# Performance work log

Measured on AMD Instinct MI355X. Metric: run time of the kernel, lower is better.

Reference implementation:

```python
import jax, jax.numpy as jnp
import numpy as np

# QuantumConv2d from ESPCN-PyTorch (quantum variant).
# QuantumLinear(kH, kW, ...) is a parameterized quantum circuit mapping a flattened
# kH*kW patch to kH Z-expectation values. We model the standard single-qubit-per-row
# RY-chain circuit: out[k] = cos( sum_w patch[k, w] + theta[k] )  (Z expectation after
# sequential RY rotations by the kW row inputs plus one trainable angle per row).
# The conv then averages the kH outputs and sums over input channels, exactly as the
# torch forward does. We replicate the original's circuits[i*j] indexing (i=out ch,
# j=in ch), and use cos(a+b)=cos a cos b - sin a sin b to turn the channel/row
# reduction into two dense einsums (same math, efficient expression).

KH, KW = 3, 3
PH, PW = 1, 1
OC = 32


def setup_inputs() -> dict:
    key = jax.random.key(0)
    k1, k2 = jax.random.split(key)
    x = jax.random.normal(k1, (8, 16, 128, 128), dtype=jnp.float32)
    # one circuit per (out_ch, in_ch, kernel_row): oC*iC*kH = 32*16*3 = 1536, kH params each
    theta = jax.random.normal(k2, (OC * 16 * KH, KH), dtype=jnp.float32)
    return {"x": x, "theta": theta}


def _row_window_sums(x):
    # x: (n, iC, H, W) -> (n, iC, kH, oH, oW): sum over the kW window for each kernel row
    xp = jnp.pad(x, ((0, 0), (0, 0), (PH, PH), (PW, PW)))
    Hp, Wp = xp.shape[2], xp.shape[3]
    oH, oW = Hp - (KH - 1), Wp - (KW - 1)
    rows = []
    for k in range(KH):  # tiny fixed loop over kernel rows
        s = xp[:, :, k:k + oH, 0:oW]
        for w in range(1, KW):
            s = s + xp[:, :, k:k + oH, w:w + oW]
        rows.append(s)
    return jnp.stack(rows, axis=2)


def reference(x, theta):
    n, iC = x.shape[0], x.shape[1]
    R = _row_window_sums(x)  # (n, iC, kH, oH, oW) angle sums per patch row
    # replicate torch's self.circuits[i * j] lookup
    idx = jnp.arange(OC)[:, None] * jnp.arange(iC)[None, :]  # (oC, iC)
    th = theta[idx]  # (oC, iC, kH)
    # out[n,i,h,w] = sum_j mean_k cos(R[n,j,k,h,w] + th[i,j,k])
    out = (jnp.einsum('njkhw,ijk->nihw', jnp.cos(R), jnp.cos(th))
           - jnp.einsum('njkhw,ijk->nihw', jnp.sin(R), jnp.sin(th))) / KH
    return out
```

## Files before the change

kernel.cpp:

```cpp
#include <hip/hip_runtime.h>

#define OC 32
#define IC 16
#define HH 128
#define WW 128
#define NB 8
#define RP 130
#define PLANE (RP * WW)
#define TRIG_DW (NB * IC * PLANE)
#define A_OFF TRIG_DW
#define A_DW (OC * 48)
#define TOTAL_DW (TRIG_DW + A_DW)

typedef __attribute__((ext_vector_type(8))) __bf16 bf16x8;
typedef __attribute__((ext_vector_type(4))) float f32x4;

#define INV_2PI 0.15915494309189535f

__device__ inline unsigned int pack2bf(float lo, float hi) {
    union { __bf16 h[2]; unsigned int u; } p;
    p.h[0] = (__bf16)lo;
    p.h[1] = (__bf16)hi;
    return p.u;
}

__device__ inline void hw_sincos(float rad, float* sn, float* cs) {
    float rev = rad * INV_2PI;
    float fr = rev - floorf(rev);
    *sn = __builtin_amdgcn_sinf(fr);
    *cs = __builtin_amdgcn_cosf(fr);
}

__global__ void trig_kernel(const float* __restrict__ x,
                            const float* __restrict__ theta,
                            unsigned int* __restrict__ ws) {
    int idx = blockIdx.x * 256 + threadIdx.x;
    if (idx >= TOTAL_DW) return;

    if (idx < TRIG_DW) {
        int w = idx & (WW - 1);
        int rowidx = idx >> 7;
        int rp = rowidx % RP;
        int pj = rowidx / RP;
        unsigned int pk;
        int r = rp - 1;
        if (r >= 0 && r < HH) {
            const float* row = x + ((size_t)pj * HH + r) * WW;
            float c0 = row[w];
            float cm = (w > 0)      ? row[w - 1] : 0.f;
            float cp = (w < WW - 1) ? row[w + 1] : 0.f;
            float s = cm + c0 + cp;
            float sn, cs;
            hw_sincos(s, &sn, &cs);
            pk = pack2bf(cs, sn);
        } else {
            pk = 0x00003F80u;
        }
        ws[idx] = pk;
    } else {
        int q = idx - A_OFF;
        int oc = q / 48;
        int m = q - oc * 48;
        int j = m / 3;
        int kk = m - 3 * j;
        float th = theta[(oc * j) * 3 + kk];
        float sn, cs;
        hw_sincos(th, &sn, &cs);
        const float inv3 = 1.0f / 3.0f;
        ws[idx] = pack2bf(cs * inv3, -sn * inv3);
    }
}

__global__ __launch_bounds__(256, 4) void gemm_kernel(
        const unsigned int* __restrict__ ws,
        float* __restrict__ out) {
    const int tx = threadIdx.x;
    const int ty = threadIdx.y;

    const int bid = blockIdx.x;
    const int wbase = (bid & 1) * 64;
    const int hp = (bid >> 1) & 63;
    const int n  = bid >> 7;
    const int h0 = hp * 2;

    const int l15 = tx & 15;
    const int lk  = tx >> 4;

    const unsigned int* At = ws + A_OFF;

    union U4 { unsigned int u[4]; bf16x8 h; };
    bf16x8 afr[3][2];
#pragma unroll
    for (int Kt = 0; Kt < 3; ++Kt)
#pragma unroll
        for (int Mt = 0; Mt < 2; ++Mt) {
            U4 a;
            const unsigned int* p = At + (l15 + 16 * Mt) * 48 + Kt * 16 + lk * 4;
#pragma unroll
            for (int e = 0; e < 4; ++e) a.u[e] = p[e];
            afr[Kt][Mt] = a.h;
        }

    bf16x8 bfr[3][2];
#pragma unroll
    for (int Nt = 0; Nt < 2; ++Nt) {
        int px = ty * 32 + 16 * Nt + l15;
        int hrow = px >> 6;
        int w = wbase + (px & 63);
        const unsigned int* base = ws + (size_t)n * IC * PLANE + w;
#pragma unroll
        for (int Kt = 0; Kt < 3; ++Kt) {
            U4 b;
#pragma unroll
            for (int e = 0; e < 4; ++e) {
                int m = Kt * 16 + lk * 4 + e;
                int j = m / 3;
                int kk = m - 3 * j;
                int rp = h0 + hrow + kk;
                b.u[e] = base[(size_t)j * PLANE + rp * WW];
            }
            bfr[Kt][Nt] = b.h;
        }
    }

    f32x4 acc[2][2];
#pragma unroll
    for (int a = 0; a < 2; ++a)
#pragma unroll
        for (int b = 0; b < 2; ++b) acc[a][b] = (f32x4){0.f, 0.f, 0.f, 0.f};

#pragma unroll
    for (int Kt = 0; Kt < 3; ++Kt)
#pragma unroll
        for (int Mt = 0; Mt < 2; ++Mt)
#pragma unroll
            for (int Nt = 0; Nt < 2; ++Nt)
                acc[Mt][Nt] = __builtin_amdgcn_mfma_f32_16x16x32_bf16(
                    afr[Kt][Mt], bfr[Kt][Nt], acc[Mt][Nt], 0, 0, 0);

#pragma unroll
    for (int Mt = 0; Mt < 2; ++Mt)
#pragma unroll
        for (int Nt = 0; Nt < 2; ++Nt)
#pragma unroll
            for (int e = 0; e < 4; ++e) {
                int oc = 16 * Mt + lk * 4 + e;
                int px = ty * 32 + 16 * Nt + l15;
                int hrow = px >> 6, wloc = px & 63;
                out[(((size_t)n * OC + oc) * HH + (h0 + hrow)) * WW + (wbase + wloc)]
                    = acc[Mt][Nt][e];
            }
}

extern "C" void kernel_launch(void* const* d_in, const int* in_sizes, int n_in,
                              void* d_out, int out_size, void* d_ws, size_t ws_size,
                              hipStream_t stream) {
    const float* x     = (const float*)d_in[0];
    const float* theta = (const float*)d_in[1];
    float* out = (float*)d_out;
    unsigned int* ws = (unsigned int*)d_ws;

    trig_kernel<<<(TOTAL_DW + 255) / 256, 256, 0, stream>>>(x, theta, ws);

    dim3 block(64, 4, 1);
    gemm_kernel<<<NB * (HH / 2) * 2, block, 0, stream>>>(ws, out);
}
```

Baseline: 74.37 us.

## Store trig workspace channel-innermost so GEMM B fragments load as 128-bit vectors

The trig workspace changes from channel-major planes (n, j, row, w) to a channel-innermost layout (n, row, w, j), and the K ordering of the A matrix changes from (j, kk) to (kk, j). Each MFMA B fragment then becomes four contiguous dwords, so it loads with one 128-bit access instead of four scattered dword gathers across planes, and A loads are vectorised too. In exchange the trig kernel now reads x with a stride across channels for consecutive threads, which may hurt coalescing of its input reads.

```diff
diff --git a/kernel.cpp b/kernel.cpp
--- a/kernel.cpp
+++ b/kernel.cpp
@@ -6,14 +6,14 @@
 #define WW 128
 #define NB 8
 #define RP 130
-#define PLANE (RP * WW)
-#define TRIG_DW (NB * IC * PLANE)
+#define TRIG_DW (NB * RP * WW * IC)
 #define A_OFF TRIG_DW
 #define A_DW (OC * 48)
 #define TOTAL_DW (TRIG_DW + A_DW)
 
 typedef __attribute__((ext_vector_type(8))) __bf16 bf16x8;
 typedef __attribute__((ext_vector_type(4))) float f32x4;
+typedef __attribute__((ext_vector_type(4))) unsigned int u32x4;
 
 #define INV_2PI 0.15915494309189535f
 
@@ -38,14 +38,15 @@
     if (idx >= TOTAL_DW) return;
 
     if (idx < TRIG_DW) {
-        int w = idx & (WW - 1);
-        int rowidx = idx >> 7;
-        int rp = rowidx % RP;
-        int pj = rowidx / RP;
-        unsigned int pk;
-        int r = rp - 1;
+        int j  = idx & 15;
+        int w  = (idx >> 4) & (WW - 1);
+        int t3 = idx >> 11;
+        int rp = t3 % RP;
+        int n  = t3 / RP;
+        int r  = rp - 1;
+        unsigned int pk = 0x00003F80u;
         if (r >= 0 && r < HH) {
-            const float* row = x + ((size_t)pj * HH + r) * WW;
+            const float* row = x + ((size_t)(n * IC + j) * HH + r) * WW;
             float c0 = row[w];
             float cm = (w > 0)      ? row[w - 1] : 0.f;
             float cp = (w < WW - 1) ? row[w + 1] : 0.f;
@@ -53,16 +54,14 @@
             float sn, cs;
             hw_sincos(s, &sn, &cs);
             pk = pack2bf(cs, sn);
-        } else {
-            pk = 0x00003F80u;
         }
         ws[idx] = pk;
     } else {
-        int q = idx - A_OFF;
+        int q  = idx - A_OFF;
         int oc = q / 48;
-        int m = q - oc * 48;
-        int j = m / 3;
-        int kk = m - 3 * j;
+        int mp = q - oc * 48;
+        int kk = mp >> 4;
+        int j  = mp & 15;
         float th = theta[(oc * j) * 3 + kk];
         float sn, cs;
         hw_sincos(th, &sn, &cs);
@@ -86,18 +85,15 @@
     const int l15 = tx & 15;
     const int lk  = tx >> 4;
 
-    const unsigned int* At = ws + A_OFF;
+    union U4 { u32x4 v; bf16x8 h; };
 
-    union U4 { unsigned int u[4]; bf16x8 h; };
     bf16x8 afr[3][2];
 #pragma unroll
     for (int Kt = 0; Kt < 3; ++Kt)
 #pragma unroll
         for (int Mt = 0; Mt < 2; ++Mt) {
             U4 a;
-            const unsigned int* p = At + (l15 + 16 * Mt) * 48 + Kt * 16 + lk * 4;
-#pragma unroll
-            for (int e = 0; e < 4; ++e) a.u[e] = p[e];
+            a.v = *(const u32x4*)(ws + A_OFF + (l15 + 16 * Mt) * 48 + Kt * 16 + lk * 4);
             afr[Kt][Mt] = a.h;
         }
 
@@ -107,18 +103,11 @@
         int px = ty * 32 + 16 * Nt + l15;
         int hrow = px >> 6;
         int w = wbase + (px & 63);
-        const unsigned int* base = ws + (size_t)n * IC * PLANE + w;
 #pragma unroll
         for (int Kt = 0; Kt < 3; ++Kt) {
+            int rp = h0 + hrow + Kt;
             U4 b;
-#pragma unroll
-            for (int e = 0; e < 4; ++e) {
-                int m = Kt * 16 + lk * 4 + e;
-                int j = m / 3;
-                int kk = m - 3 * j;
-                int rp = h0 + hrow + kk;
-                b.u[e] = base[(size_t)j * PLANE + rp * WW];
-            }
+            b.v = *(const u32x4*)(ws + ((size_t)(n * RP + rp) * WW + w) * 16 + lk * 4);
             bfr[Kt][Nt] = b.h;
         }
     }
```

Result: slower. 81.96 us (+10.2%).
